# Performance work log

Hardware: AMD Instinct MI355X
Metric: run time of the kernel (lower is better)

The kernel has to match this reference:

```python
import jax, jax.numpy as jnp
import numpy as np

N_NODES = 50000
N_EDGES = 800000
N_GRAPHS = 128
IN_CH = 16
IN_CTX = 16
H_G = 128
H_C = 128
H_F = 128


def _lin_init(key, fan_in, fan_out):
    k1, k2 = jax.random.split(key)
    s = 1.0 / np.sqrt(fan_in)
    W = jax.random.uniform(k1, (fan_in, fan_out), minval=-s, maxval=s, dtype=jnp.float32)
    b = jax.random.uniform(k2, (fan_out,), minval=-s, maxval=s, dtype=jnp.float32)
    return W, b


def setup_inputs() -> dict:
    key = jax.random.key(0)
    ks = jax.random.split(key, 16)
    inp = {}
    inp['x'] = jax.random.normal(ks[0], (N_NODES, IN_CH), dtype=jnp.float32)
    inp['x_context'] = jax.random.normal(ks[1], (N_GRAPHS, IN_CTX), dtype=jnp.float32)
    inp['edge_index'] = jax.random.randint(ks[2], (2, N_EDGES), 0, N_NODES, dtype=jnp.int64)
    inp['batch'] = jnp.sort(jax.random.randint(ks[3], (N_NODES,), 0, N_GRAPHS, dtype=jnp.int64))
    inp['edge_weight'] = jax.random.uniform(ks[4], (N_EDGES,), dtype=jnp.float32)
    # graph conv weights (GCNConv): layer0 [IN_CH,H_G], layers1-3 [H_G,H_G]
    dims = [(IN_CH, H_G), (H_G, H_G), (H_G, H_G), (H_G, H_G)]
    for i, (di, do) in enumerate(dims):
        W, b = _lin_init(ks[5 + i], di, do)
        inp[f'gW{i}'] = W
        inp[f'gb{i}'] = b
    # context FC: [IN_CTX,H_C], [H_C,H_C], [H_C,H_C]
    cdims = [(IN_CTX, H_C), (H_C, H_C), (H_C, H_C)]
    for i, (di, do) in enumerate(cdims):
        W, b = _lin_init(ks[9 + i], di, do)
        inp[f'cW{i}'] = W
        inp[f'cb{i}'] = b
    # fc stack: [H_G+H_C,H_F], [H_F,H_F], [H_F,H_F]
    fdims = [(H_G + H_C, H_F), (H_F, H_F), (H_F, H_F)]
    for i, (di, do) in enumerate(fdims):
        W, b = _lin_init(ks[12 + i], di, do)
        inp[f'fW{i}'] = W
        inp[f'fb{i}'] = b
    return inp


def _forward(x, x_context, edge_index, batch, edge_weight,
             gWs, gbs, cWs, cbs, fWs, fbs):
    n = x.shape[0]
    src, dst = edge_index[0], edge_index[1]
    loop = jnp.arange(n, dtype=edge_index.dtype)
    # GCN: add self-loops with weight 1, symmetric normalization
    src_f = jnp.concatenate([src, loop])
    dst_f = jnp.concatenate([dst, loop])
    ew_f = jnp.concatenate([edge_weight, jnp.ones((n,), dtype=edge_weight.dtype)])
    deg = jax.ops.segment_sum(ew_f, dst_f, num_segments=n)
    dinv = jnp.where(deg > 0, jax.lax.rsqrt(jnp.where(deg > 0, deg, 1.0)), 0.0)
    norm = dinv[src_f] * ew_f * dinv[dst_f]  # [E+N]

    h = x
    for W, b in zip(gWs, gbs):
        hw = h @ W                                   # [N, H_G]
        msg = norm[:, None] * hw[src_f]              # gather + scale
        h = jax.ops.segment_sum(msg, dst_f, num_segments=n) + b
        h = jax.nn.relu(h)

    # global mean pool over graphs
    s = jax.ops.segment_sum(h, batch, num_segments=N_GRAPHS)
    cnt = jax.ops.segment_sum(jnp.ones((n,), dtype=h.dtype), batch, num_segments=N_GRAPHS)
    g = s / jnp.maximum(cnt, 1.0)[:, None]           # [G, H_G]

    c = x_context
    for W, b in zip(cWs, cbs):
        c = jax.nn.relu(c @ W + b)

    z = jnp.concatenate([g, c], axis=-1)             # [G, H_G + H_C]
    for W, b in zip(fWs[:-1], fbs[:-1]):
        z = jax.nn.relu(z @ W + b)
    z = z @ fWs[-1] + fbs[-1]
    return z


def reference(x, x_context, edge_index, batch, edge_weight,
              gW0, gb0, gW1, gb1, gW2, gb2, gW3, gb3,
              cW0, cb0, cW1, cb1, cW2, cb2,
              fW0, fb0, fW1, fb1, fW2, fb2):
    return _forward(x, x_context, edge_index, batch, edge_weight,
                    [gW0, gW1, gW2, gW3], [gb0, gb1, gb2, gb3],
                    [cW0, cW1, cW2], [cb0, cb1, cb2],
                    [fW0, fW1, fW2], [fb0, fb1, fb2])
```

## Files before the change

kernel.cpp:

```cpp
#include <hip/hip_runtime.h>

typedef __attribute__((ext_vector_type(8))) short short8;
typedef __attribute__((ext_vector_type(4))) float f32x4;

#define IN_CH 16
#define CAP 64

__device__ inline unsigned int bf16_rne(float f) {
  unsigned int u = __float_as_uint(f);
  unsigned int r = u + 0x7fffu + ((u >> 16) & 1u);
  return r >> 16;
}
__device__ inline float bf16lo(unsigned int g) { return __uint_as_float(g << 16); }
__device__ inline float bf16hi(unsigned int g) { return __uint_as_float(g & 0xffff0000u); }
__device__ inline short8 as_short8(uint4 u) {
  union { uint4 u; short8 s; } cv; cv.u = u; return cv.s;
}

__global__ void zero_kernel(int* __restrict__ cnt, int n) {
  int i = blockIdx.x * blockDim.x + threadIdx.x;
  for (int j = i; j < n; j += gridDim.x * blockDim.x) cnt[j] = 0;
}

__global__ void build_kernel(const int* __restrict__ ei, const float* __restrict__ ew,
                             int* __restrict__ cnt, int2* __restrict__ bucket, int E) {
  int e = blockIdx.x * blockDim.x + threadIdx.x;
  if (e < E) {
    int dst = ei[E + e];
    int old = atomicAdd(&cnt[dst], 1);
    if (old < CAP) {
      int2 p;
      p.x = ei[e];
      p.y = __float_as_int(ew[e]);
      bucket[(size_t)dst * CAP + old] = p;
    }
  }
}

__global__ __launch_bounds__(256) void node_prep_kernel(
    const int* __restrict__ cnt, const int2* __restrict__ bucket,
    const float* __restrict__ x, float* __restrict__ dinv,
    float* __restrict__ xs, int n) {
  int lane = threadIdx.x & 15;
  int v = blockIdx.x * 16 + (threadIdx.x >> 4);
  if (v >= n) return;
  int c = min(cnt[v], CAP);
  float s = 0.f;
  for (int j = lane; j < c; j += 16)
    s += __int_as_float(bucket[(size_t)v * CAP + j].y);
#pragma unroll
  for (int off = 1; off < 16; off <<= 1) s += __shfl_xor(s, off);
  float dv = rsqrtf(1.0f + s);
  if (lane == 0) dinv[v] = dv;
  xs[(size_t)v * 16 + lane] = dv * x[(size_t)v * 16 + lane];
}

__global__ __launch_bounds__(256) void spmm16_kernel(
    const float4* __restrict__ xs4, const float* __restrict__ dinv,
    const int* __restrict__ cnt, const int2* __restrict__ bucket,
    float4* __restrict__ A0_4, int n) {
  const int l = threadIdx.x & 63;
  const int q = l >> 2;
  const int c4 = l & 3;
  const int v = (blockIdx.x << 2) + (threadIdx.x >> 6);
  if (v >= n) return;
  const size_t beg = (size_t)v * CAP;
  const int c = min(cnt[v], CAP);
  float4 s = make_float4(0.f, 0.f, 0.f, 0.f);
  for (int j = 0; j < c; j += 16) {
    int jj = j + q;
    bool ok = jj < c;
    int2 p = bucket[ok ? beg + jj : beg];
    float w = ok ? __int_as_float(p.y) : 0.f;
    float4 u = xs4[(size_t)p.x * 4 + c4];
    s.x += w * u.x; s.y += w * u.y; s.z += w * u.z; s.w += w * u.w;
  }
#pragma unroll
  for (int off = 4; off < 64; off <<= 1) {
    s.x += __shfl_xor(s.x, off);
    s.y += __shfl_xor(s.y, off);
    s.z += __shfl_xor(s.z, off);
    s.w += __shfl_xor(s.w, off);
  }
  float dv = dinv[v];
  float4 self = xs4[(size_t)v * 4 + c4];
  if (q == 0) {
    float4 o;
    o.x = dv * (s.x + self.x);
    o.y = dv * (s.y + self.y);
    o.z = dv * (s.z + self.z);
    o.w = dv * (s.w + self.w);
    A0_4[(size_t)v * 4 + c4] = o;
  }
}

__global__ __launch_bounds__(256) void spmm_bf16_kernel(
    const uint4* __restrict__ Hs4, const float* __restrict__ dinv,
    const int* __restrict__ cnt, const int2* __restrict__ bucket,
    uint4* __restrict__ Ab4, int n) {
  const int l = threadIdx.x & 63;
  const int q = l >> 4;
  const int c16 = l & 15;
  const int v = (blockIdx.x << 2) + (threadIdx.x >> 6);
  if (v >= n) return;
  const size_t beg = (size_t)v * CAP;
  const int c = min(cnt[v], CAP);
  float s[8] = {};
  for (int j = 0; j < c; j += 16) {
#pragma unroll
    for (int i = 0; i < 4; ++i) {
      int jj = j + i * 4 + q;
      bool ok = jj < c;
      int2 p = bucket[ok ? beg + jj : beg];
      float w = ok ? __int_as_float(p.y) : 0.f;
      uint4 u = Hs4[(size_t)p.x * 16 + c16];
      s[0] += w * bf16lo(u.x); s[1] += w * bf16hi(u.x);
      s[2] += w * bf16lo(u.y); s[3] += w * bf16hi(u.y);
      s[4] += w * bf16lo(u.z); s[5] += w * bf16hi(u.z);
      s[6] += w * bf16lo(u.w); s[7] += w * bf16hi(u.w);
    }
  }
#pragma unroll
  for (int j = 0; j < 8; ++j) {
    s[j] += __shfl_xor(s[j], 16);
    s[j] += __shfl_xor(s[j], 32);
  }
  float dv = dinv[v];
  uint4 self = Hs4[(size_t)v * 16 + c16];
  float r0 = dv * (s[0] + bf16lo(self.x));
  float r1 = dv * (s[1] + bf16hi(self.x));
  float r2 = dv * (s[2] + bf16lo(self.y));
  float r3 = dv * (s[3] + bf16hi(self.y));
  float r4 = dv * (s[4] + bf16lo(self.z));
  float r5 = dv * (s[5] + bf16hi(self.z));
  float r6 = dv * (s[6] + bf16lo(self.w));
  float r7 = dv * (s[7] + bf16hi(self.w));
  if (q == 0) {
    uint4 o;
    o.x = bf16_rne(r0) | (bf16_rne(r1) << 16);
    o.y = bf16_rne(r2) | (bf16_rne(r3) << 16);
    o.z = bf16_rne(r4) | (bf16_rne(r5) << 16);
    o.w = bf16_rne(r6) | (bf16_rne(r7) << 16);
    Ab4[(size_t)v * 16 + c16] = o;
  }
}

__global__ __launch_bounds__(256) void gemm16_kernel(
    const float* __restrict__ X, const float* __restrict__ W,
    const float* __restrict__ bias, const float* __restrict__ dinv,
    unsigned int* __restrict__ Hb, int n) {
  __shared__ float Ws[16][128];
  __shared__ float Xs[32][16];
  const int tid = threadIdx.x;
  const int row0 = blockIdx.x * 32;

  for (int i = tid * 4; i < 16 * 128; i += 1024)
    *(float4*)&Ws[0][i] = *(const float4*)&W[i];
  for (int i = tid * 4; i < 32 * 16; i += 1024) {
    int r = i / 16, k = i % 16;
    int rr = row0 + r;
    float4 v = make_float4(0.f, 0.f, 0.f, 0.f);
    if (rr < n) v = *(const float4*)&X[(size_t)rr * 16 + k];
    *(float4*)&Xs[r][k] = v;
  }
  __syncthreads();

  const int tc = (tid & 31) * 4;
  const int tr = (tid >> 5) * 4;
  float acc[4][4] = {};
  for (int k = 0; k < 16; k += 4) {
    float4 xv[4];
#pragma unroll
    for (int r = 0; r < 4; ++r) xv[r] = *(const float4*)&Xs[tr + r][k];
    float4 wv[4];
#pragma unroll
    for (int kk = 0; kk < 4; ++kk) wv[kk] = *(const float4*)&Ws[k + kk][tc];
#pragma unroll
    for (int r = 0; r < 4; ++r) {
      float xr[4] = {xv[r].x, xv[r].y, xv[r].z, xv[r].w};
#pragma unroll
      for (int kk = 0; kk < 4; ++kk) {
        acc[r][0] += xr[kk] * wv[kk].x;
        acc[r][1] += xr[kk] * wv[kk].y;
        acc[r][2] += xr[kk] * wv[kk].z;
        acc[r][3] += xr[kk] * wv[kk].w;
      }
    }
  }

  float4 bv = *(const float4*)&bias[tc];
#pragma unroll
  for (int r = 0; r < 4; ++r) {
    int rr = row0 + tr + r;
    if (rr < n) {
      float dv = dinv[rr];
      float o0 = dv * fmaxf(acc[r][0] + bv.x, 0.f);
      float o1 = dv * fmaxf(acc[r][1] + bv.y, 0.f);
      float o2 = dv * fmaxf(acc[r][2] + bv.z, 0.f);
      float o3 = dv * fmaxf(acc[r][3] + bv.w, 0.f);
      uint2 st;
      st.x = bf16_rne(o0) | (bf16_rne(o1) << 16);
      st.y = bf16_rne(o2) | (bf16_rne(o3) << 16);
      *(uint2*)&Hb[(size_t)rr * 64 + (tc >> 1)] = st;
    }
  }
}

__global__ void prep_wt3_kernel(const float* __restrict__ W1, const float* __restrict__ W2,
                                const float* __restrict__ W3, unsigned int* __restrict__ Wt) {
  int gid = blockIdx.x * 256 + threadIdx.x;
  if (gid >= 3 * 128 * 64) return;
  int layer = gid >> 13;
  int idx = gid & 8191;
  const float* W = (layer == 0) ? W1 : (layer == 1) ? W2 : W3;
  int c = idx >> 6, kp = idx & 63;
  float f0 = W[(2 * kp) * 128 + c];
  float f1 = W[(2 * kp + 1) * 128 + c];
  Wt[gid] = bf16_rne(f0) | (bf16_rne(f1) << 16);
}

__global__ __launch_bounds__(256) void gemm_mfma_kernel(
    const unsigned int* __restrict__ Ab, const unsigned int* __restrict__ Wtb,
    const float* __restrict__ bias, const float* __restrict__ dinv, int scale_out,
    unsigned short* __restrict__ Hh, int n) {
  __shared__ unsigned int Wlds[128 * 68];
  const int tid = threadIdx.x;
  for (int idx = tid; idx < 128 * 16; idx += 256) {
    int row = idx >> 4, slot = idx & 15;
    uint4 v = ((const uint4*)Wtb)[idx];
    *(uint4*)&Wlds[row * 68 + slot * 4] = v;
  }
  __syncthreads();

  const int lane = tid & 63, wid = tid >> 6;
  const int r0 = blockIdx.x * 128 + wid * 32;
  const int rowA = r0 + (lane & 15);
  const int kgrp = lane >> 4;
  const uint4* Abase = (const uint4*)Ab;

  f32x4 acc[2][8] = {};
#pragma unroll
  for (int kstep = 0; kstep < 4; ++kstep) {
    short8 a[2];
#pragma unroll
    for (int rb = 0; rb < 2; ++rb)
      a[rb] = as_short8(Abase[(size_t)(rowA + rb * 16) * 16 + kstep * 4 + kgrp]);
#pragma unroll
    for (int cb = 0; cb < 8; ++cb) {
      short8 b = as_short8(*(const uint4*)&Wlds[(cb * 16 + (lane & 15)) * 68 + (kstep * 4 + kgrp) * 4]);
      acc[0][cb] = __builtin_amdgcn_mfma_f32_16x16x32_bf16(a[0], b, acc[0][cb], 0, 0, 0);
      acc[1][cb] = __builtin_amdgcn_mfma_f32_16x16x32_bf16(a[1], b, acc[1][cb], 0, 0, 0);
    }
  }

  const int rbase = kgrp * 4;
  float dsc[2][4];
#pragma unroll
  for (int rb = 0; rb < 2; ++rb)
#pragma unroll
    for (int i = 0; i < 4; ++i) {
      int row = r0 + rb * 16 + rbase + i;
      dsc[rb][i] = (scale_out && row < n) ? dinv[row] : 1.0f;
    }

#pragma unroll
  for (int cb = 0; cb < 8; ++cb) {
    int col = cb * 16 + (lane & 15);
    float bv = bias[col];
#pragma unroll
    for (int rb = 0; rb < 2; ++rb) {
#pragma unroll
      for (int i = 0; i < 4; ++i) {
        int row = r0 + rb * 16 + rbase + i;
        if (row < n) {
          float o = dsc[rb][i] * fmaxf(acc[rb][cb][i] + bv, 0.f);
          Hh[(size_t)row * 128 + col] = (unsigned short)bf16_rne(o);
        }
      }
    }
  }
}

__global__ __launch_bounds__(256) void pool_ctx_head_kernel(
    const unsigned int* __restrict__ Hb, const int* __restrict__ batch,
    const float* __restrict__ xc,
    const float* __restrict__ cW0, const float* __restrict__ cb0,
    const float* __restrict__ cW1, const float* __restrict__ cb1,
    const float* __restrict__ cW2, const float* __restrict__ cb2,
    const float* __restrict__ fW0, const float* __restrict__ fb0,
    const float* __restrict__ fW1, const float* __restrict__ fb1,
    const float* __restrict__ fW2, const float* __restrict__ fb2,
    float* __restrict__ out, int n) {
  int g = blockIdx.x;
  int lo = 0, hi = n;
  while (lo < hi) { int mid = (lo + hi) >> 1; if (batch[mid] < g) lo = mid + 1; else hi = mid; }
  int start = lo;
  lo = start; hi = n;
  while (lo < hi) { int mid = (lo + hi) >> 1; if (batch[mid] < g + 1) lo = mid + 1; else hi = mid; }
  int end = lo;

  int lane = threadIdx.x & 63, grp = threadIdx.x >> 6;
  float s0 = 0.f, s1 = 0.f;
  for (int v = start + grp; v < end; v += 4) {
    unsigned int u = Hb[((size_t)v << 6) + lane];
    s0 += bf16lo(u);
    s1 += bf16hi(u);
  }
  __shared__ float red[4][128];
  red[grp][2 * lane] = s0;
  red[grp][2 * lane + 1] = s1;

  __shared__ float xin[16];
  __shared__ float z[256];
  __shared__ float buf[128];
  int c = threadIdx.x;
  if (c < 16) xin[c] = xc[g * 16 + c];
  __syncthreads();

  if (c < 128) {
    float t = red[0][c] + red[1][c] + red[2][c] + red[3][c];
    z[c] = t / fmaxf((float)(end - start), 1.0f);
  }
  if (c < 128) {
    float a = cb0[c];
#pragma unroll
    for (int k = 0; k < 16; ++k) a += xin[k] * cW0[k * 128 + c];
    buf[c] = fmaxf(a, 0.f);
  }
  __syncthreads();
  float a1 = 0.f;
  if (c < 128) {
    a1 = cb1[c];
    for (int k = 0; k < 128; ++k) a1 += buf[k] * cW1[k * 128 + c];
    a1 = fmaxf(a1, 0.f);
  }
  __syncthreads();
  if (c < 128) buf[c] = a1;
  __syncthreads();
  if (c < 128) {
    float a2 = cb2[c];
    for (int k = 0; k < 128; ++k) a2 += buf[k] * cW2[k * 128 + c];
    z[128 + c] = fmaxf(a2, 0.f);
  }
  __syncthreads();
  float h0 = 0.f;
  if (c < 128) {
    h0 = fb0[c];
    for (int k = 0; k < 256; ++k) h0 += z[k] * fW0[k * 128 + c];
    h0 = fmaxf(h0, 0.f);
  }
  __syncthreads();
  if (c < 128) buf[c] = h0;
  __syncthreads();
  float h1 = 0.f;
  if (c < 128) {
    h1 = fb1[c];
    for (int k = 0; k < 128; ++k) h1 += buf[k] * fW1[k * 128 + c];
    h1 = fmaxf(h1, 0.f);
  }
  __syncthreads();
  if (c < 128) buf[c] = h1;
  __syncthreads();
  if (c < 128) {
    float h2 = fb2[c];
    for (int k = 0; k < 128; ++k) h2 += buf[k] * fW2[k * 128 + c];
    out[g * 128 + c] = h2;
  }
}

extern "C" void kernel_launch(void* const* d_in, const int* in_sizes, int n_in,
                              void* d_out, int out_size, void* d_ws, size_t ws_size,
                              hipStream_t stream) {
  const float* x     = (const float*)d_in[0];
  const float* xc    = (const float*)d_in[1];
  const int*   ei    = (const int*)d_in[2];
  const int*   batch = (const int*)d_in[3];
  const float* ew    = (const float*)d_in[4];
  const float* gW[4] = {(const float*)d_in[5], (const float*)d_in[7], (const float*)d_in[9],  (const float*)d_in[11]};
  const float* gb[4] = {(const float*)d_in[6], (const float*)d_in[8], (const float*)d_in[10], (const float*)d_in[12]};
  const float* cW0 = (const float*)d_in[13]; const float* cb0 = (const float*)d_in[14];
  const float* cW1 = (const float*)d_in[15]; const float* cb1 = (const float*)d_in[16];
  const float* cW2 = (const float*)d_in[17]; const float* cb2 = (const float*)d_in[18];
  const float* fW0 = (const float*)d_in[19]; const float* fb0 = (const float*)d_in[20];
  const float* fW1 = (const float*)d_in[21]; const float* fb1 = (const float*)d_in[22];
  const float* fW2 = (const float*)d_in[23]; const float* fb2 = (const float*)d_in[24];
  float* out = (float*)d_out;

  const int N = in_sizes[3];
  const int E = in_sizes[4];
  const int G = in_sizes[1] / IN_CH;
  const int Np = (N + 127) & ~127;

  char* p = (char*)d_ws;
  auto alloc = [&](size_t bytes) { char* r = p; p += (bytes + 255) & ~(size_t)255; return r; };
  int*   cnt    = (int*)  alloc((size_t)N * 4);
  int2*  bucket = (int2*) alloc((size_t)N * CAP * 8);
  float* dinv   = (float*)alloc((size_t)N * 4);
  float* xs     = (float*)alloc((size_t)N * 16 * 4);
  float* A0     = (float*)alloc((size_t)N * 16 * 4);
  unsigned int* Ab = (unsigned int*)alloc((size_t)Np * 64 * 4);
  unsigned int* Hb = (unsigned int*)alloc((size_t)Np * 64 * 4);
  unsigned int* Wt = (unsigned int*)alloc((size_t)3 * 128 * 64 * 4);

  int nbE = (E + 255) / 256;

  zero_kernel<<<128, 256, 0, stream>>>(cnt, N);
  build_kernel<<<nbE, 256, 0, stream>>>(ei, ew, cnt, bucket, E);
  node_prep_kernel<<<(N + 15) / 16, 256, 0, stream>>>(cnt, bucket, x, dinv, xs, N);

  prep_wt3_kernel<<<96, 256, 0, stream>>>(gW[1], gW[2], gW[3], Wt);

  spmm16_kernel<<<(N + 3) / 4, 256, 0, stream>>>((const float4*)xs, dinv, cnt, bucket,
                                                 (float4*)A0, N);
  gemm16_kernel<<<(N + 31) / 32, 256, 0, stream>>>(A0, gW[0], gb[0], dinv, Hb, N);

  for (int l = 0; l < 3; ++l) {
    spmm_bf16_kernel<<<(N + 3) / 4, 256, 0, stream>>>((const uint4*)Hb, dinv, cnt, bucket,
                                                      (uint4*)Ab, N);
    gemm_mfma_kernel<<<Np / 128, 256, 0, stream>>>(Ab, Wt + (size_t)l * 8192, gb[l + 1], dinv,
                                                   (l < 2) ? 1 : 0, (unsigned short*)Hb, N);
  }

  pool_ctx_head_kernel<<<G, 256, 0, stream>>>(Hb, batch, xc, cW0, cb0, cW1, cb1, cW2, cb2,
                                              fW0, fb0, fW1, fb1, fW2, fb2, out, N);
}
```

Before: 293.6 us.

## Split pooling into multi-block partial sums and stage MLP weights through LDS

Global mean pooling moves into its own kernel that uses four blocks per graph, each writing partial sums to a workspace buffer, so more blocks share the bandwidth-bound reduction. A second kernel combines the partials and runs the context and head MLPs. Each layer first copies its weight matrix into a 128 KB LDS array with float4 loads, and all 256 threads work by splitting the K dimension in half. This adds a kernel launch and large LDS use, which limits occupancy to one block per CU, in exchange for more parallelism in pooling and all threads active in the MLPs.

After: 302.7 us. 1.03x slower.

```diff
diff --git a/kernel.cpp b/kernel.cpp
--- a/kernel.cpp
+++ b/kernel.cpp
@@ -281,8 +281,57 @@
   }
 }
 
-__global__ __launch_bounds__(256) void pool_ctx_head_kernel(
+__global__ __launch_bounds__(256) void pool_part_kernel(
     const unsigned int* __restrict__ Hb, const int* __restrict__ batch,
+    float* __restrict__ gpp, int G, int n) {
+  int b = blockIdx.x;
+  int g = b >> 2, chunk = b & 3;
+  int lo = 0, hi = n;
+  while (lo < hi) { int mid = (lo + hi) >> 1; if (batch[mid] < g) lo = mid + 1; else hi = mid; }
+  int start = lo;
+  lo = start; hi = n;
+  while (lo < hi) { int mid = (lo + hi) >> 1; if (batch[mid] < g + 1) lo = mid + 1; else hi = mid; }
+  int end = lo;
+
+  int lane = threadIdx.x & 63, grp = threadIdx.x >> 6;
+  float s0 = 0.f, s1 = 0.f;
+  for (int v = start + chunk * 4 + grp; v < end; v += 16) {
+    unsigned int u = Hb[((size_t)v << 6) + lane];
+    s0 += bf16lo(u);
+    s1 += bf16hi(u);
+  }
+  __shared__ float red[4][128];
+  red[grp][2 * lane] = s0;
+  red[grp][2 * lane + 1] = s1;
+  __syncthreads();
+  if (threadIdx.x < 128) {
+    float t = red[0][threadIdx.x] + red[1][threadIdx.x] + red[2][threadIdx.x] + red[3][threadIdx.x];
+    gpp[((size_t)chunk * G + g) * 128 + threadIdx.x] = t;
+  }
+}
+
+__device__ inline void mlp_layer(const float* __restrict__ Wg, const float* __restrict__ bg,
+                                 const float* in_lds, float* out_lds, float* Wl,
+                                 float (*psum)[128], int K, int tid, int do_relu) {
+  __syncthreads();
+  for (int i = tid * 4; i < K * 128; i += 1024)
+    *(float4*)&Wl[i] = *(const float4*)&Wg[i];
+  __syncthreads();
+  int h = tid >> 7, c = tid & 127;
+  int k0 = h * (K >> 1), k1 = k0 + (K >> 1);
+  float s = 0.f;
+#pragma unroll 4
+  for (int k = k0; k < k1; ++k) s += in_lds[k] * Wl[k * 128 + c];
+  psum[h][c] = s;
+  __syncthreads();
+  if (tid < 128) {
+    float r = psum[0][c] + psum[1][c] + bg[c];
+    out_lds[c] = do_relu ? fmaxf(r, 0.f) : r;
+  }
+}
+
+__global__ __launch_bounds__(256) void ctx_head_kernel(
+    const float* __restrict__ gpp, const int* __restrict__ batch,
     const float* __restrict__ xc,
     const float* __restrict__ cW0, const float* __restrict__ cb0,
     const float* __restrict__ cW1, const float* __restrict__ cb1,
@@ -290,81 +339,52 @@
     const float* __restrict__ fW0, const float* __restrict__ fb0,
     const float* __restrict__ fW1, const float* __restrict__ fb1,
     const float* __restrict__ fW2, const float* __restrict__ fb2,
-    float* __restrict__ out, int n) {
+    float* __restrict__ out, int G, int n) {
+  __shared__ float Wl[256 * 128];
+  __shared__ float zz[256];
+  __shared__ float tA[128];
+  __shared__ float tB[128];
+  __shared__ float psum[2][128];
+  __shared__ float xin[16];
+
   int g = blockIdx.x;
+  int tid = threadIdx.x;
+
   int lo = 0, hi = n;
   while (lo < hi) { int mid = (lo + hi) >> 1; if (batch[mid] < g) lo = mid + 1; else hi = mid; }
   int start = lo;
   lo = start; hi = n;
   while (lo < hi) { int mid = (lo + hi) >> 1; if (batch[mid] < g + 1) lo = mid + 1; else hi = mid; }
   int end = lo;
-
-  int lane = threadIdx.x & 63, grp = threadIdx.x >> 6;
-  float s0 = 0.f, s1 = 0.f;
-  for (int v = start + grp; v < end; v += 4) {
-    unsigned int u = Hb[((size_t)v << 6) + lane];
-    s0 += bf16lo(u);
-    s1 += bf16hi(u);
-  }
-  __shared__ float red[4][128];
-  red[grp][2 * lane] = s0;
-  red[grp][2 * lane + 1] = s1;
-
-  __shared__ float xin[16];
-  __shared__ float z[256];
-  __shared__ float buf[128];
-  int c = threadIdx.x;
-  if (c < 16) xin[c] = xc[g * 16 + c];
-  __syncthreads();
-
-  if (c < 128) {
-    float t = red[0][c] + red[1][c] + red[2][c] + red[3][c];
-    z[c] = t / fmaxf((float)(end - start), 1.0f);
-  }
-  if (c < 128) {
-    float a = cb0[c];
-#pragma unroll
-    for (int k = 0; k < 16; ++k) a += xin[k] * cW0[k * 128 + c];
-    buf[c] = fmaxf(a, 0.f);
-  }
-  __syncthreads();
-  float a1 = 0.f;
-  if (c < 128) {
-    a1 = cb1[c];
-    for (int k = 0; k < 128; ++k) a1 += buf[k] * cW1[k * 128 + c];
-    a1 = fmaxf(a1, 0.f);
-  }
-  __syncthreads();
-  if (c < 128) buf[c] = a1;
-  __syncthreads();
-  if (c < 128) {
-    float a2 = cb2[c];
-    for (int k = 0; k < 128; ++k) a2 += buf[k] * cW2[k * 128 + c];
-    z[128 + c] = fmaxf(a2, 0.f);
-  }
-  __syncthreads();
-  float h0 = 0.f;
-  if (c < 128) {
-    h0 = fb0[c];
-    for (int k = 0; k < 256; ++k) h0 += z[k] * fW0[k * 128 + c];
-    h0 = fmaxf(h0, 0.f);
-  }
-  __syncthreads();
-  if (c < 128) buf[c] = h0;
-  __syncthreads();
-  float h1 = 0.f;
-  if (c < 128) {
-    h1 = fb1[c];
-    for (int k = 0; k < 128; ++k) h1 += buf[k] * fW1[k * 128 + c];
-    h1 = fmaxf(h1, 0.f);
-  }
-  __syncthreads();
-  if (c < 128) buf[c] = h1;
-  __syncthreads();
-  if (c < 128) {
-    float h2 = fb2[c];
-    for (int k = 0; k < 128; ++k) h2 += buf[k] * fW2[k * 128 + c];
-    out[g * 128 + c] = h2;
+  float inv_cnt = 1.0f / fmaxf((float)(end - start), 1.0f);
+
+  if (tid < 128) {
+    float t = gpp[((size_t)0 * G + g) * 128 + tid] + gpp[((size_t)1 * G + g) * 128 + tid] +
+              gpp[((size_t)2 * G + g) * 128 + tid] + gpp[((size_t)3 * G + g) * 128 + tid];
+    zz[tid] = t * inv_cnt;
+  }
+  if (tid < 16) xin[tid] = xc[g * 16 + tid];
+
+  mlp_layer(cW0, cb0, xin, tA, Wl, psum, 16, tid, 1);
+  mlp_layer(cW1, cb1, tA, tB, Wl, psum, 128, tid, 1);
+  mlp_layer(cW2, cb2, tB, zz + 128, Wl, psum, 128, tid, 1);
+  mlp_layer(fW0, fb0, zz, tA, Wl, psum, 256, tid, 1);
+  mlp_layer(fW1, fb1, tA, tB, Wl, psum, 128, tid, 1);
+  __syncthreads();
+  for (int i = tid * 4; i < 128 * 128; i += 1024)
+    *(float4*)&Wl[i] = *(const float4*)&fW2[i];
+  __syncthreads();
+  {
+    int h = tid >> 7, c = tid & 127;
+    int k0 = h * 64, k1 = k0 + 64;
+    float s = 0.f;
+#pragma unroll 4
+    for (int k = k0; k < k1; ++k) s += tB[k] * Wl[k * 128 + c];
+    psum[h][c] = s;
+  }
+  __syncthreads();
+  if (tid < 128) {
+    out[g * 128 + tid] = psum[0][tid] + psum[1][tid] + fb2[tid];
   }
 }
 
@@ -401,6 +421,7 @@
   unsigned int* Ab = (unsigned int*)alloc((size_t)Np * 64 * 4);
   unsigned int* Hb = (unsigned int*)alloc((size_t)Np * 64 * 4);
   unsigned int* Wt = (unsigned int*)alloc((size_t)3 * 128 * 64 * 4);
+  float* gpp = (float*)alloc((size_t)4 * G * 128 * 4);
 
   int nbE = (E + 255) / 256;
 
@@ -421,6 +442,7 @@
                                                    (l < 2) ? 1 : 0, (unsigned short*)Hb, N);
   }
 
-  pool_ctx_head_kernel<<<G, 256, 0, stream>>>(Hb, batch, xc, cW0, cb0, cW1, cb1, cW2, cb2,
-                                              fW0, fb0, fW1, fb1, fW2, fb2, out, N);
-}
+  pool_part_kernel<<<4 * G, 256, 0, stream>>>(Hb, batch, gpp, G, N);
+  ctx_head_kernel<<<G, 256, 0, stream>>>(gpp, batch, xc, cW0, cb0, cW1, cb1, cW2, cb2,
+                                         fW0, fb0, fW1, fb1, fW2, fb2, out, G, N);
+}
```
